# Kernel optimization log

Measured on AMD Instinct MI355X. Metric: run time of the kernel, lower is better.

## Reference

```python
import jax, jax.numpy as jnp
import numpy as np

EMBED_DIM = 256
NUM_HEADS = 8


def positional_encoding(max_seq_len, embed_dim):
    # Faithful to torch source: exponent uses 2*i/embed_dim with raw column index i;
    # row 0 is all zeros; sin on even cols, cos on odd cols for rows 1:.
    pos = jnp.arange(max_seq_len, dtype=jnp.float32)[:, None]          # [L,1]
    i = jnp.arange(embed_dim, dtype=jnp.float32)[None, :]              # [1,D]
    angles = pos / jnp.power(10000.0, 2.0 * i / embed_dim)             # [L,D]
    pe = jnp.where((jnp.arange(embed_dim) % 2 == 0)[None, :],
                   jnp.sin(angles), jnp.cos(angles))
    pe = pe.at[0].set(0.0)
    return pe


def setup_inputs() -> dict:
    key = jax.random.key(0)
    ks = jax.random.split(key, 9)
    b, c, h, w = 4, EMBED_DIM, 48, 48
    d = EMBED_DIM  # internal_dim (downsample_rate=1)
    s = 1.0 / np.sqrt(d)
    inp = {
        "x": jax.random.normal(ks[0], (b, c, h, w), dtype=jnp.float32),
        "wq": jax.random.uniform(ks[1], (d, d), jnp.float32, -s, s),
        "bq": jax.random.uniform(ks[2], (d,), jnp.float32, -s, s),
        "wk": jax.random.uniform(ks[3], (d, d), jnp.float32, -s, s),
        "bk": jax.random.uniform(ks[4], (d,), jnp.float32, -s, s),
        "wv": jax.random.uniform(ks[5], (d, d), jnp.float32, -s, s),
        "bv": jax.random.uniform(ks[6], (d,), jnp.float32, -s, s),
        "wo": jax.random.uniform(ks[7], (d, d), jnp.float32, -s, s),
        "bo": jax.random.uniform(ks[8], (d,), jnp.float32, -s, s),
    }
    return inp


def reference(x, wq, bq, wk, bk, wv, bv, wo, bo):
    b, c, h, w = x.shape
    n = h * w
    H = NUM_HEADS
    dh = c // H
    xs = x.reshape(b, c, n).transpose(0, 2, 1)            # [b, n, c]
    xs = xs + positional_encoding(n, c)[None]             # add PE
    q = xs @ wq.T + bq                                    # [b, n, c]
    k = xs @ wk.T + bk
    v = xs @ wv.T + bv
    # separate heads -> [b, H, n, dh]
    q = q.reshape(b, n, H, dh).transpose(0, 2, 1, 3)
    k = k.reshape(b, n, H, dh).transpose(0, 2, 1, 3)
    v = v.reshape(b, n, H, dh).transpose(0, 2, 1, 3)
    attn = jnp.einsum("bhqd,bhkd->bhqk", q, k) / jnp.sqrt(jnp.float32(dh))
    attn = jax.nn.softmax(attn, axis=-1)
    out = jnp.einsum("bhqk,bhkd->bhqd", attn, v)          # [b, H, n, dh]
    out = out.transpose(0, 2, 1, 3).reshape(b, n, c)      # recombine heads
    out = out @ wo.T + bo                                 # out_proj
    return out.transpose(0, 2, 1).reshape(b, c, h, w)
```

## Files before the change

### kernel.cpp

```cpp
#include <hip/hip_runtime.h>

#define EMBED 256
#define NPOS  2304
#define BATCH 4
#define NH    8
#define DH    32

typedef float f32x4  __attribute__((ext_vector_type(4)));
typedef short bf16x8 __attribute__((ext_vector_type(8)));
typedef short s16x4  __attribute__((ext_vector_type(4)));
typedef unsigned u32x4 __attribute__((ext_vector_type(4)));

static __device__ __forceinline__ short f2b(float f) {
    union { float f; unsigned u; } c; c.f = f;
    unsigned r = (c.u + 0x7FFFu + ((c.u >> 16) & 1u)) >> 16;
    return (short)r;
}

static __device__ __forceinline__ unsigned cvtpk(float lo, float hi) {
    unsigned r;
    asm("v_cvt_pk_bf16_f32 %0, %1, %2" : "=v"(r) : "v"(lo), "v"(hi));
    return r;
}

static __device__ __forceinline__ float fexp2(float x) {
    float r;
    asm("v_exp_f32 %0, %1" : "=v"(r) : "v"(x));
    return r;
}

static __device__ __forceinline__ void plswap32(unsigned& a, unsigned& b) {
    asm("v_permlane32_swap_b32 %0, %1" : "+v"(a), "+v"(b));
}
static __device__ __forceinline__ void plswap16(unsigned& a, unsigned& b) {
    asm("v_permlane16_swap_b32 %0, %1" : "+v"(a), "+v"(b));
}

static __device__ __forceinline__ void gl_lds16(const short* g, short* l) {
    __builtin_amdgcn_global_load_lds(
        (const __attribute__((address_space(1))) unsigned int*)(g),
        (__attribute__((address_space(3))) unsigned int*)(l),
        16, 0, 0);
}

__global__ __launch_bounds__(256) void prep_all(
        const float* __restrict__ x,
        const float* __restrict__ wq, const float* __restrict__ wk,
        const float* __restrict__ wv, const float* __restrict__ wo,
        short* __restrict__ wqkv, short* __restrict__ wob,
        short* __restrict__ xs) {
    __shared__ float xt[32][65];
    int blk = blockIdx.x;
    int t = threadIdx.x;
    if (blk < 1024) {
        int g = blk * 256 + t;
        if (g < 196608) {
            int j = g >> 8, kk = g & 255;
            int proj = j >> 8, jj = j & 255;
            const float* s = (proj == 0) ? wq : (proj == 1) ? wk : wv;
            wqkv[g] = f2b(s[jj * 256 + kk]);
        } else if (g < 262144) {
            int h2 = g - 196608;
            wob[h2] = f2b(wo[h2]);
        }
        return;
    }
    int bx = blk - 1024;
    int b = bx / 288, rem = bx % 288;
    int c0 = (rem / 36) * 32, pos0 = (rem % 36) * 64;
    int j = t & 63, i0 = t >> 6;
    const float* xp = x + (size_t)(b * EMBED + c0) * NPOS + pos0;
#pragma unroll
    for (int rr = 0; rr < 8; ++rr) {
        int i = rr * 4 + i0;
        xt[i][j] = xp[(size_t)i * NPOS + j];
    }
    __syncthreads();
    int ii = (t & 15) * 2, jj0 = t >> 4;
    const float kln = -0.07195578415606394f;
#pragma unroll
    for (int pp = 0; pp < 4; ++pp) {
        int jj = pp * 16 + jj0;
        int pos = pos0 + jj;
        float v0 = xt[ii][jj], v1 = xt[ii + 1][jj];
        float pe0 = 0.f, pe1 = 0.f;
        if (pos > 0) {
            int c = c0 + ii;
            float a0 = (float)pos * __expf((float)c * kln);
            float a1 = (float)pos * __expf((float)(c + 1) * kln);
            pe0 = __sinf(a0);
            pe1 = __cosf(a1);
        }
        unsigned lo = (unsigned short)f2b(v0 + pe0);
        unsigned hi = (unsigned short)f2b(v1 + pe1);
        *reinterpret_cast<unsigned*>(xs + (size_t)(b * NPOS + pos) * EMBED + c0 + ii) =
            lo | (hi << 16);
    }
}

__global__ __launch_bounds__(256) void gemm_qkv(
        const short* __restrict__ A, const short* __restrict__ Bw,
        const float* __restrict__ bq, const float* __restrict__ bk,
        const float* __restrict__ bv,
        short* __restrict__ qd, short* __restrict__ kd, short* __restrict__ vtd) {
    __shared__ short a_sm[64 * 32];
    __shared__ short b_sm[64 * 32];
    int bx = blockIdx.x;
    int bm = bx / 12, bn = bx % 12;
    int m0 = bm * 64, n0 = bn * 64;
    int t = threadIdx.x;
    int lane = t & 63, wid = t >> 6;
    int wm = wid >> 1, wn = wid & 1;
    int l15 = lane & 15, l4 = lane >> 4;

    f32x4 acc[2][2];
#pragma unroll
    for (int ni = 0; ni < 2; ++ni) {
        int jcol = n0 + wn * 32 + ni * 16 + l15;
        int proj = jcol >> 8, jj = jcol & 255;
        float bias = ((proj == 0) ? bq : (proj == 1) ? bk : bv)[jj];
        f32x4 bi = {bias, bias, bias, bias};
        acc[0][ni] = bi;
        acc[1][ni] = bi;
    }

    int srow = t >> 2, sblk = t & 3;
    int ssw = (sblk ^ ((srow >> 1) & 3)) * 8;
    const short* ag = &A[(size_t)(m0 + srow) * 256 + sblk * 8];
    const short* bg = &Bw[(size_t)(n0 + srow) * 256 + sblk * 8];
    short* al = &a_sm[srow * 32 + ssw];
    short* bl = &b_sm[srow * 32 + ssw];

    for (int ks = 0; ks < 8; ++ks) {
        __syncthreads();
        *(bf16x8*)al = *(const bf16x8*)(ag + ks * 32);
        *(bf16x8*)bl = *(const bf16x8*)(bg + ks * 32);
        __syncthreads();
        bf16x8 af[2], bf[2];
#pragma unroll
        for (int mi = 0; mi < 2; ++mi) {
            int ar = wm * 32 + mi * 16 + l15;
            af[mi] = *(const bf16x8*)&a_sm[ar * 32 + ((l4 ^ ((ar >> 1) & 3)) * 8)];
        }
#pragma unroll
        for (int ni = 0; ni < 2; ++ni) {
            int br = wn * 32 + ni * 16 + l15;
            bf[ni] = *(const bf16x8*)&b_sm[br * 32 + ((l4 ^ ((br >> 1) & 3)) * 8)];
        }
#pragma unroll
        for (int mi = 0; mi < 2; ++mi)
#pragma unroll
            for (int ni = 0; ni < 2; ++ni)
                acc[mi][ni] = __builtin_amdgcn_mfma_f32_16x16x32_bf16(
                    af[mi], bf[ni], acc[mi][ni], 0, 0, 0);
    }

    const float qs = 0.2550348623f;
#pragma unroll
    for (int mi = 0; mi < 2; ++mi) {
        int rowb = m0 + wm * 32 + mi * 16 + l4 * 4;
        int b = rowb / NPOS;
        int pos = rowb - b * NPOS;
#pragma unroll
        for (int ni = 0; ni < 2; ++ni) {
            int jcol = n0 + wn * 32 + ni * 16 + l15;
            int proj = jcol >> 8, jj = jcol & 255;
            int h = jj >> 5, d = jj & 31;
            if (proj == 2) {
                s16x4 pk;
#pragma unroll
                for (int r = 0; r < 4; ++r) pk[r] = f2b(acc[mi][ni][r]);
                *(s16x4*)&vtd[((size_t)(b * NH + h) * DH + d) * NPOS + pos] = pk;
            } else {
                short* dst = (proj == 0) ? qd : kd;
                float sc = (proj == 0) ? qs : 1.0f;
#pragma unroll
                for (int r = 0; r < 4; ++r)
                    dst[((size_t)(b * NH + h) * NPOS + pos + r) * DH + d] =
                        f2b(acc[mi][ni][r] * sc);
            }
        }
    }
}


__global__ __launch_bounds__(256) void attn_fwd(
        const short* __restrict__ Q, const short* __restrict__ K,
        const short* __restrict__ VT, short* __restrict__ AO) {
    __shared__ short smem[16384];

    int bx0 = blockIdx.x;
    int bx = (bx0 & 7) * 288 + (bx0 >> 3);
    int bh = bx / 72, qg = bx % 72;
    int q0 = qg * 32;
    int t = threadIdx.x, lane = t & 63, wid = t >> 6;
    int l15 = lane & 15, l4 = lane >> 4;

    const short* Qb = Q + ((size_t)bh * NPOS + q0) * DH;
    bf16x8 qf[2];
    qf[0] = *(const bf16x8*)&Qb[l15 * DH + l4 * 8];
    qf[1] = *(const bf16x8*)&Qb[(16 + l15) * DH + l4 * 8];

    int kv0 = wid * 576;
    int ra = lane >> 2, blk = lane & 3;
    int swzk = (ra >> 1) & 3;
    int swzv = (ra & 3) ^ ((ra >> 2) & 3);
    const short* kga = K + ((size_t)bh * NPOS + kv0 + ra) * DH + ((blk ^ swzk) * 8);
    const short* vga = VT + ((size_t)bh * DH + ra) * NPOS + kv0 + ((blk ^ swzv) * 8);

    short* kbuf = smem + wid * 4096;
    short* vbuf = kbuf + 2048;

#pragma unroll
    for (int p = 0; p < 2; ++p) {
        gl_lds16(kga + p * 1024,            kbuf + p * 1024);
        gl_lds16(kga + p * 1024 + 16 * DH,  kbuf + p * 1024 + 512);
        gl_lds16(vga + p * 32,              vbuf + p * 1024);
        gl_lds16(vga + p * 32 + 16 * NPOS,  vbuf + p * 1024 + 512);
    }

    f32x4 zero = {0.f, 0.f, 0.f, 0.f};
    f32x4 o[2][2];
    o[0][0] = zero; o[0][1] = zero; o[1][0] = zero; o[1][1] = zero;
    float ls[2] = {0.f, 0.f};
    const float MB = -17.312340490667561f;
    const f32x4 mb = {MB, MB, MB, MB};

    int kswr = (l4 ^ ((l15 >> 1) & 3)) * 8;
    int vswr = (l4 ^ ((l15 & 3) ^ ((l15 >> 2) & 3))) * 8;

#pragma unroll 1
    for (int tt = 0; tt < 18; ++tt) {
        int buf = tt & 1;
        if (tt < 17) asm volatile("s_waitcnt vmcnt(4)" ::: "memory");
        else         asm volatile("s_waitcnt vmcnt(0)" ::: "memory");
        __builtin_amdgcn_s_barrier();

        const short* kb = kbuf + buf * 1024;
        const short* vb = vbuf + buf * 1024;
        bf16x8 kf0 = *(const bf16x8*)&kb[l15 * 32 + kswr];
        bf16x8 kf1 = *(const bf16x8*)&kb[(16 + l15) * 32 + kswr];
        bf16x8 vf0 = *(const bf16x8*)&vb[l15 * 32 + vswr];
        bf16x8 vf1 = *(const bf16x8*)&vb[(16 + l15) * 32 + vswr];
        asm volatile("s_waitcnt lgkmcnt(0)" ::: "memory");
        __builtin_amdgcn_sched_barrier(0);

        if (tt + 2 < 18) {
            gl_lds16(kga + (tt + 2) * 1024,            kbuf + buf * 1024);
            gl_lds16(kga + (tt + 2) * 1024 + 16 * DH,  kbuf + buf * 1024 + 512);
            gl_lds16(vga + (tt + 2) * 32,              vbuf + buf * 1024);
            gl_lds16(vga + (tt + 2) * 32 + 16 * NPOS,  vbuf + buf * 1024 + 512);
        }

#pragma unroll
        for (int qt = 0; qt < 2; ++qt) {
            f32x4 s0 = __builtin_amdgcn_mfma_f32_16x16x32_bf16(kf0, qf[qt], mb, 0, 0, 0);
            f32x4 s1 = __builtin_amdgcn_mfma_f32_16x16x32_bf16(kf1, qf[qt], mb, 0, 0, 0);

            float e00 = fexp2(s0[0]), e01 = fexp2(s0[1]), e02 = fexp2(s0[2]), e03 = fexp2(s0[3]);
            float e10 = fexp2(s1[0]), e11 = fexp2(s1[1]), e12 = fexp2(s1[2]), e13 = fexp2(s1[3]);
            ls[qt] += ((e00 + e01) + (e02 + e03)) + ((e10 + e11) + (e12 + e13));

            unsigned p00 = cvtpk(e00, e01), p01 = cvtpk(e02, e03);
            unsigned p10 = cvtpk(e10, e11), p11 = cvtpk(e12, e13);
            unsigned a0 = p00, b0 = p10;
            plswap32(a0, b0); plswap16(a0, b0);
            unsigned a1 = p01, b1 = p11;
            plswap32(a1, b1); plswap16(a1, b1);
            u32x4 fr = {a0, a1, b0, b1};
            bf16x8 pf = __builtin_bit_cast(bf16x8, fr);

            o[0][qt] = __builtin_amdgcn_mfma_f32_16x16x32_bf16(vf0, pf, o[0][qt], 0, 0, 0);
            o[1][qt] = __builtin_amdgcn_mfma_f32_16x16x32_bf16(vf1, pf, o[1][qt], 0, 0, 0);
        }
    }

#pragma unroll
    for (int qt = 0; qt < 2; ++qt) {
        ls[qt] += __shfl_xor(ls[qt], 16);
        ls[qt] += __shfl_xor(ls[qt], 32);
    }

    if (wid > 0) {
        f32x4* od = (f32x4*)(smem + wid * 4096);
        float* ld = (float*)(smem + wid * 4096 + 2048);
#pragma unroll
        for (int qt = 0; qt < 2; ++qt) {
            ld[qt * 64 + lane] = ls[qt];
#pragma unroll
            for (int dt = 0; dt < 2; ++dt)
                od[(qt * 2 + dt) * 64 + lane] = o[dt][qt];
        }
    }
    __syncthreads();
    if (wid == 0) {
        int b = bh >> 3, h = bh & 7;
#pragma unroll
        for (int qt = 0; qt < 2; ++qt) {
            float lt = ls[qt];
#pragma unroll
            for (int w = 1; w < 4; ++w)
                lt += ((float*)(smem + w * 4096 + 2048))[qt * 64 + lane];
            float inv = __builtin_amdgcn_rcpf(lt);
            int qrow = q0 + qt * 16 + l15;
            size_t obase = ((size_t)b * NPOS + qrow) * EMBED + h * DH;
#pragma unroll
            for (int dt = 0; dt < 2; ++dt) {
                f32x4 ot = o[dt][qt];
#pragma unroll
                for (int w = 1; w < 4; ++w)
                    ot += ((f32x4*)(smem + w * 4096))[(qt * 2 + dt) * 64 + lane];
                unsigned x0 = cvtpk(ot[0] * inv, ot[1] * inv);
                unsigned x1 = cvtpk(ot[2] * inv, ot[3] * inv);
                *(unsigned long long*)&AO[obase + dt * 16 + l4 * 4] =
                    (unsigned long long)x0 | ((unsigned long long)x1 << 32);
            }
        }
    }
}

__global__ __launch_bounds__(256) void gemm_out(
        const short* __restrict__ A, const short* __restrict__ Bw,
        const float* __restrict__ bo, float* __restrict__ out) {
    __shared__ short a_sm[32 * 32];
    __shared__ short b_sm[64 * 32];
    int bx = blockIdx.x;
    int bm = bx >> 2, bn = bx & 3;
    int m0 = bm * 32, n0 = bn * 64;
    int t = threadIdx.x;
    int lane = t & 63, wid = t >> 6;
    int wm = wid >> 1, wn = wid & 1;
    int l15 = lane & 15, l4 = lane >> 4;

    f32x4 acc[2];
#pragma unroll
    for (int ni = 0; ni < 2; ++ni) {
        float bias = bo[n0 + wn * 32 + ni * 16 + l15];
        f32x4 bi = {bias, bias, bias, bias};
        acc[ni] = bi;
    }

    int srow = t >> 2, sblk = t & 3;
    int ssw = (sblk ^ ((srow >> 1) & 3)) * 8;
    const short* ag = &A[(size_t)(m0 + srow) * 256 + sblk * 8];
    const short* bg = &Bw[(size_t)(n0 + srow) * 256 + sblk * 8];
    short* al = &a_sm[srow * 32 + ssw];
    short* bl = &b_sm[srow * 32 + ssw];

    for (int ks = 0; ks < 8; ++ks) {
        __syncthreads();
        if (t < 128) *(bf16x8*)al = *(const bf16x8*)(ag + ks * 32);
        *(bf16x8*)bl = *(const bf16x8*)(bg + ks * 32);
        __syncthreads();
        int ar = wm * 16 + l15;
        bf16x8 af = *(const bf16x8*)&a_sm[ar * 32 + ((l4 ^ ((ar >> 1) & 3)) * 8)];
        bf16x8 bf[2];
#pragma unroll
        for (int ni = 0; ni < 2; ++ni) {
            int br = wn * 32 + ni * 16 + l15;
            bf[ni] = *(const bf16x8*)&b_sm[br * 32 + ((l4 ^ ((br >> 1) & 3)) * 8)];
        }
#pragma unroll
        for (int ni = 0; ni < 2; ++ni)
            acc[ni] = __builtin_amdgcn_mfma_f32_16x16x32_bf16(af, bf[ni], acc[ni], 0, 0, 0);
    }

    int rowb = m0 + wm * 16 + l4 * 4;
    int b = rowb / NPOS;
    int pos = rowb - b * NPOS;
#pragma unroll
    for (int ni = 0; ni < 2; ++ni) {
        int jcol = n0 + wn * 32 + ni * 16 + l15;
        *(f32x4*)&out[((size_t)(b * EMBED) + jcol) * NPOS + pos] = acc[ni];
    }
}

extern "C" void kernel_launch(void* const* d_in, const int* in_sizes, int n_in,
                              void* d_out, int out_size, void* d_ws, size_t ws_size,
                              hipStream_t stream) {
    const float* x  = (const float*)d_in[0];
    const float* wq = (const float*)d_in[1];
    const float* bq = (const float*)d_in[2];
    const float* wk = (const float*)d_in[3];
    const float* bk = (const float*)d_in[4];
    const float* wv = (const float*)d_in[5];
    const float* bv = (const float*)d_in[6];
    const float* wo = (const float*)d_in[7];
    const float* bo = (const float*)d_in[8];

    char* ws = (char*)d_ws;
    short* wqkv = (short*)(ws);
    short* wob  = (short*)(ws + 393216);
    short* xs   = (short*)(ws + 524288);
    short* qb   = (short*)(ws + 5242880);
    short* kb   = (short*)(ws + 9961472);
    short* vtb  = (short*)(ws + 14680064);
    short* ao   = (short*)(ws + 19398656);
    float* out  = (float*)d_out;

    hipLaunchKernelGGL(prep_all, dim3(2176), dim3(256), 0, stream,
                       x, wq, wk, wv, wo, wqkv, wob, xs);
    hipLaunchKernelGGL(gemm_qkv, dim3(1728), dim3(256), 0, stream,
                       xs, wqkv, bq, bk, bv, qb, kb, vtb);
    hipLaunchKernelGGL(attn_fwd, dim3(2304), dim3(256), 0, stream, qb, kb, vtb, ao);
    hipLaunchKernelGGL(gemm_out, dim3(1152), dim3(256), 0, stream, ao, wob, bo, out);
}
```

Measured before the change: 74.28 us.

## Load K/V fragments directly from global memory instead of LDS staging

Replaces the double-buffered global-to-LDS async loads of K and V tiles (with swizzle, waitcnt and barriers) with direct per-lane vector loads from global memory into registers, unrolled by two. LDS is now used only for the cross-wave reduction of partial outputs and row sums, which shrinks the shared memory footprint. This removes the per-iteration barrier and LDS round trip, but relies on the compiler and caches to hide global load latency without explicit prefetching.

```diff
diff --git a/kernel.cpp b/kernel.cpp
--- a/kernel.cpp
+++ b/kernel.cpp
@@ -34,13 +34,6 @@
 }
 static __device__ __forceinline__ void plswap16(unsigned& a, unsigned& b) {
     asm("v_permlane16_swap_b32 %0, %1" : "+v"(a), "+v"(b));
-}
-
-static __device__ __forceinline__ void gl_lds16(const short* g, short* l) {
-    __builtin_amdgcn_global_load_lds(
-        (const __attribute__((address_space(1))) unsigned int*)(g),
-        (__attribute__((address_space(3))) unsigned int*)(l),
-        16, 0, 0);
 }
 
 __global__ __launch_bounds__(256) void prep_all(
@@ -187,7 +180,8 @@
 __global__ __launch_bounds__(256) void attn_fwd(
         const short* __restrict__ Q, const short* __restrict__ K,
         const short* __restrict__ VT, short* __restrict__ AO) {
-    __shared__ short smem[16384];
+    __shared__ f32x4 osm[3][4][64];
+    __shared__ float lsm[3][2][64];
 
     int bx0 = blockIdx.x;
     int bx = (bx0 & 7) * 288 + (bx0 >> 3);
@@ -202,22 +196,8 @@
     qf[1] = *(const bf16x8*)&Qb[(16 + l15) * DH + l4 * 8];
 
     int kv0 = wid * 576;
-    int ra = lane >> 2, blk = lane & 3;
-    int swzk = (ra >> 1) & 3;
-    int swzv = (ra & 3) ^ ((ra >> 2) & 3);
-    const short* kga = K + ((size_t)bh * NPOS + kv0 + ra) * DH + ((blk ^ swzk) * 8);
-    const short* vga = VT + ((size_t)bh * DH + ra) * NPOS + kv0 + ((blk ^ swzv) * 8);
-
-    short* kbuf = smem + wid * 4096;
-    short* vbuf = kbuf + 2048;
-
-#pragma unroll
-    for (int p = 0; p < 2; ++p) {
-        gl_lds16(kga + p * 1024,            kbuf + p * 1024);
-        gl_lds16(kga + p * 1024 + 16 * DH,  kbuf + p * 1024 + 512);
-        gl_lds16(vga + p * 32,              vbuf + p * 1024);
-        gl_lds16(vga + p * 32 + 16 * NPOS,  vbuf + p * 1024 + 512);
-    }
+    const short* kptr = K + ((size_t)bh * NPOS + kv0 + l15) * DH + l4 * 8;
+    const short* vptr = VT + ((size_t)bh * DH + l15) * NPOS + kv0 + l4 * 8;
 
     f32x4 zero = {0.f, 0.f, 0.f, 0.f};
     f32x4 o[2][2];
@@ -226,31 +206,12 @@
     const float MB = -17.312340490667561f;
     const f32x4 mb = {MB, MB, MB, MB};
 
-    int kswr = (l4 ^ ((l15 >> 1) & 3)) * 8;
-    int vswr = (l4 ^ ((l15 & 3) ^ ((l15 >> 2) & 3))) * 8;
-
-#pragma unroll 1
+#pragma unroll 2
     for (int tt = 0; tt < 18; ++tt) {
-        int buf = tt & 1;
-        if (tt < 17) asm volatile("s_waitcnt vmcnt(4)" ::: "memory");
-        else         asm volatile("s_waitcnt vmcnt(0)" ::: "memory");
-        __builtin_amdgcn_s_barrier();
-
-        const short* kb = kbuf + buf * 1024;
-        const short* vb = vbuf + buf * 1024;
-        bf16x8 kf0 = *(const bf16x8*)&kb[l15 * 32 + kswr];
-        bf16x8 kf1 = *(const bf16x8*)&kb[(16 + l15) * 32 + kswr];
-        bf16x8 vf0 = *(const bf16x8*)&vb[l15 * 32 + vswr];
-        bf16x8 vf1 = *(const bf16x8*)&vb[(16 + l15) * 32 + vswr];
-        asm volatile("s_waitcnt lgkmcnt(0)" ::: "memory");
-        __builtin_amdgcn_sched_barrier(0);
-
-        if (tt + 2 < 18) {
-            gl_lds16(kga + (tt + 2) * 1024,            kbuf + buf * 1024);
-            gl_lds16(kga + (tt + 2) * 1024 + 16 * DH,  kbuf + buf * 1024 + 512);
-            gl_lds16(vga + (tt + 2) * 32,              vbuf + buf * 1024);
-            gl_lds16(vga + (tt + 2) * 32 + 16 * NPOS,  vbuf + buf * 1024 + 512);
-        }
+        bf16x8 kf0 = *(const bf16x8*)(kptr + tt * 1024);
+        bf16x8 kf1 = *(const bf16x8*)(kptr + tt * 1024 + 512);
+        bf16x8 vf0 = *(const bf16x8*)(vptr + tt * 32);
+        bf16x8 vf1 = *(const bf16x8*)(vptr + tt * 32 + 16 * NPOS);
 
 #pragma unroll
         for (int qt = 0; qt < 2; ++qt) {
@@ -282,14 +243,12 @@
     }
 
     if (wid > 0) {
-        f32x4* od = (f32x4*)(smem + wid * 4096);
-        float* ld = (float*)(smem + wid * 4096 + 2048);
 #pragma unroll
         for (int qt = 0; qt < 2; ++qt) {
-            ld[qt * 64 + lane] = ls[qt];
+            lsm[wid - 1][qt][lane] = ls[qt];
 #pragma unroll
             for (int dt = 0; dt < 2; ++dt)
-                od[(qt * 2 + dt) * 64 + lane] = o[dt][qt];
+                osm[wid - 1][qt * 2 + dt][lane] = o[dt][qt];
         }
     }
     __syncthreads();
@@ -297,19 +256,14 @@
         int b = bh >> 3, h = bh & 7;
 #pragma unroll
         for (int qt = 0; qt < 2; ++qt) {
-            float lt = ls[qt];
-#pragma unroll
-            for (int w = 1; w < 4; ++w)
-                lt += ((float*)(smem + w * 4096 + 2048))[qt * 64 + lane];
+            float lt = ls[qt] + lsm[0][qt][lane] + lsm[1][qt][lane] + lsm[2][qt][lane];
             float inv = __builtin_amdgcn_rcpf(lt);
             int qrow = q0 + qt * 16 + l15;
             size_t obase = ((size_t)b * NPOS + qrow) * EMBED + h * DH;
 #pragma unroll
             for (int dt = 0; dt < 2; ++dt) {
-                f32x4 ot = o[dt][qt];
-#pragma unroll
-                for (int w = 1; w < 4; ++w)
-                    ot += ((f32x4*)(smem + w * 4096))[(qt * 2 + dt) * 64 + lane];
+                f32x4 ot = o[dt][qt] + osm[0][qt * 2 + dt][lane]
+                         + osm[1][qt * 2 + dt][lane] + osm[2][qt * 2 + dt][lane];
                 unsigned x0 = cvtpk(ot[0] * inv, ot[1] * inv);
                 unsigned x1 = cvtpk(ot[2] * inv, ot[3] * inv);
                 *(unsigned long long*)&AO[obase + dt * 16 + l4 * 4] =
```

New measurement: 95.44 us. 28.5% more time.
